# Kernel tuning notes

Measured on AMD Instinct MI355X. Metric: run time of the kernel, lower is better.

Reference implementation:

```python
import math
import jax, jax.numpy as jnp
import numpy as np

NUM_BUCKETS = 32
MAX_DISTANCE = 128
HEADS = 16
D_MODEL = 1024
SEQ = 1024
BATCH = 4
SCALE = (D_MODEL // HEADS) ** -0.5  # applied ONLY to the relative-position bias, per the source


def _rel_pos_bucket_causal(seq_len):
    """Causal T5 relative-position bucket: ret[i, j] for query i, key j."""
    pos = jnp.arange(seq_len)
    # rel_pos = k - q ; n = -rel_pos = q - k, clamped at 0 (causal branch)
    n = jnp.maximum(pos[:, None] - pos[None, :], 0)
    max_exact = NUM_BUCKETS // 2  # 16
    # log-spaced buckets for large distances; guard n>=1 to avoid log(0)
    val_large = max_exact + (
        jnp.log(jnp.maximum(n, 1).astype(jnp.float32) / max_exact)
        / math.log(MAX_DISTANCE / max_exact)
        * (NUM_BUCKETS - max_exact)
    ).astype(jnp.int32)
    val_large = jnp.minimum(val_large, NUM_BUCKETS - 1)
    return jnp.where(n < max_exact, n, val_large)  # [i, j] int32


def setup_inputs() -> dict:
    key = jax.random.key(0)
    ks = jax.random.split(key, 6)
    s = 0.02
    return {
        "x": jax.random.normal(ks[0], (BATCH, SEQ, D_MODEL), jnp.float32),
        "Wq": jax.random.normal(ks[1], (D_MODEL, D_MODEL), jnp.float32) * s,
        "bq": jnp.zeros((D_MODEL,), jnp.float32),
        "Wk": jax.random.normal(ks[2], (D_MODEL, D_MODEL), jnp.float32) * s,
        "bk": jnp.zeros((D_MODEL,), jnp.float32),
        "Wv": jax.random.normal(ks[3], (D_MODEL, D_MODEL), jnp.float32) * s,
        "bv": jnp.zeros((D_MODEL,), jnp.float32),
        "Wo": jax.random.normal(ks[4], (D_MODEL, D_MODEL), jnp.float32) * s,
        "bo": jnp.zeros((D_MODEL,), jnp.float32),
        "rel_emb": jax.random.normal(ks[5], (NUM_BUCKETS, HEADS), jnp.float32) * s,
    }


def reference(x, Wq, bq, Wk, bk, Wv, bv, Wo, bo, rel_emb):
    b, n, d = x.shape
    h, hd = HEADS, d // HEADS
    # projections (torch Linear: x @ W^T + b)
    q = (x @ Wq.T + bq).reshape(b, n, h, hd).transpose(0, 2, 1, 3)  # bhnd
    k = (x @ Wk.T + bk).reshape(b, n, h, hd).transpose(0, 2, 1, 3)
    v = (x @ Wv.T + bv).reshape(b, n, h, hd).transpose(0, 2, 1, 3)
    # unscaled dot-product scores (module does not scale q.k)
    sim = jnp.einsum("bhid,bhjd->bhij", q, k)
    # T5 relative-position bias, scaled by head_dim^-0.5
    rp_bucket = _rel_pos_bucket_causal(n)            # [i, j]
    bias = rel_emb[rp_bucket]                        # [i, j, h]
    sim = sim + jnp.transpose(bias, (2, 0, 1)) * SCALE  # broadcast over batch
    # additive causal mask (-inf above diagonal)
    i = jnp.arange(n)
    causal = jnp.where(i[None, :] > i[:, None], -jnp.inf, 0.0).astype(sim.dtype)
    sim = sim + causal
    attn = jax.nn.softmax(sim, axis=-1)
    out = jnp.einsum("bhij,bhjd->bhid", attn, v)
    out = out.transpose(0, 2, 1, 3).reshape(b, n, d)
    return out @ Wo.T + bo
```

## Files before the change

### kernel.cpp

```cpp
#include <hip/hip_runtime.h>
#include <hip/hip_bf16.h>
#include <stdint.h>

#define B_   4
#define SEQ_ 1024
#define DM   1024
#define H_   16
#define HD   64

typedef __bf16 bf16;
typedef __bf16 bf16x8 __attribute__((ext_vector_type(8)));
typedef __bf16 bf16x4v __attribute__((ext_vector_type(4)));
typedef float  f32x4 __attribute__((ext_vector_type(4)));

__device__ __forceinline__ void gl_lds16(const void* g, void* s_uniform) {
    __builtin_amdgcn_global_load_lds(
        (const __attribute__((address_space(1))) uint32_t*)g,
        (__attribute__((address_space(3))) uint32_t*)s_uniform,
        16, 0, 0);
}

__global__ __launch_bounds__(256) void prep_kernel(
    const float* __restrict__ x, const float* __restrict__ Wq,
    const float* __restrict__ Wk, const float* __restrict__ Wv,
    const float* __restrict__ Wo, const float* __restrict__ rel,
    bf16* __restrict__ xb, bf16* __restrict__ wqkvb, bf16* __restrict__ wob,
    float* __restrict__ biasT)
{
    int tid = blockIdx.x * 256 + threadIdx.x;
    int stride = gridDim.x * 256;

    for (int i = tid; i < (B_*SEQ_*DM)/4; i += stride) {
        float4 v = ((const float4*)x)[i];
        bf16x4v o; o[0]=(bf16)v.x; o[1]=(bf16)v.y; o[2]=(bf16)v.z; o[3]=(bf16)v.w;
        ((bf16x4v*)xb)[i] = o;
    }
    for (int i = tid; i < (3*DM*DM)/4; i += stride) {
        int n = i >> 8, k4 = i & 255;
        const float* src = (n < 1024) ? Wq : (n < 2048) ? Wk : Wv;
        float4 v = ((const float4*)(src + (size_t)(n & 1023) * DM))[k4];
        bf16x4v o; o[0]=(bf16)v.x; o[1]=(bf16)v.y; o[2]=(bf16)v.z; o[3]=(bf16)v.w;
        ((bf16x4v*)wqkvb)[i] = o;
    }
    for (int i = tid; i < (DM*DM)/4; i += stride) {
        float4 v = ((const float4*)Wo)[i];
        bf16x4v o; o[0]=(bf16)v.x; o[1]=(bf16)v.y; o[2]=(bf16)v.z; o[3]=(bf16)v.w;
        ((bf16x4v*)wob)[i] = o;
    }
    for (int i = tid; i < H_ * SEQ_; i += stride) {
        int h = i >> 10, dist = i & 1023;
        int bkt;
        if (dist < 16) {
            bkt = dist;
        } else {
            float r = logf((float)dist * (1.0f/16.0f)) / logf(8.0f) * 16.0f;
            int vb = 16 + (int)r;
            bkt = vb > 31 ? 31 : vb;
        }
        biasT[i] = rel[bkt * H_ + h] * 0.125f;
    }
}

template<int NT>
__global__ __launch_bounds__(256, 3) void gemm_ring(
    const bf16* __restrict__ Ag, const bf16* __restrict__ Bg,
    int ntx, int chunk,
    bf16* __restrict__ qb, bf16* __restrict__ kb, bf16* __restrict__ vtb,
    const float* __restrict__ bq, const float* __restrict__ bk,
    const float* __restrict__ bv)
{
    __shared__ __align__(16) bf16 tile[3][256 * 32];

    const int t = threadIdx.x;
    const int lane = t & 63, w = t >> 6;
    const int wr = w >> 1, wc = w & 1;
    const int row_l = lane & 15;
    const int lg = lane >> 4;

    int sw = (blockIdx.x & 7) * chunk + (blockIdx.x >> 3);
    int tx = sw % ntx, ty = sw / ntx;
    const int m0 = ty * 128, n0 = tx * 128;

    f32x4 acc[4][4] = {};

    auto STAGE = [&](int buf, int kt) {
        bf16* dst = &tile[buf][0];
        #pragma unroll
        for (int i = 0; i < 4; ++i) {
            int e = i * 2048 + t * 8;
            int r = e >> 5;
            int csw = ((t & 3) ^ (r & 3)) << 3;
            const bf16* src = (r < 128)
                ? (Ag + (long)(m0 + r) * 1024 + kt * 32 + csw)
                : (Bg + (long)(n0 + r - 128) * 1024 + kt * 32 + csw);
            gl_lds16(src, dst + i * 2048 + w * 512);
        }
    };

    auto COMPUTE = [&](int buf) {
        const bf16* bp = &tile[buf][0];
        bf16x8 af[4], bfr[4];
        #pragma unroll
        for (int m = 0; m < 4; ++m) {
            int ra = wr * 64 + m * 16 + row_l;
            af[m] = *(const bf16x8*)&bp[ra * 32 + ((lg ^ (ra & 3)) << 3)];
        }
        #pragma unroll
        for (int n = 0; n < 4; ++n) {
            int rb = 128 + wc * 64 + n * 16 + row_l;
            bfr[n] = *(const bf16x8*)&bp[rb * 32 + ((lg ^ (rb & 3)) << 3)];
        }
        #pragma unroll
        for (int m = 0; m < 4; ++m)
            #pragma unroll
            for (int n = 0; n < 4; ++n)
                acc[m][n] = __builtin_amdgcn_mfma_f32_16x16x32_bf16(
                    af[m], bfr[n], acc[m][n], 0, 0, 0);
    };

    STAGE(0, 0); STAGE(1, 1);
    asm volatile("s_waitcnt vmcnt(4)" ::: "memory");
    __builtin_amdgcn_s_barrier();

    int cb = 0;
    for (int kt = 0; kt < NT; ++kt) {
        int sb = cb - 1; if (sb < 0) sb += 3;
        if (kt + 2 < NT) STAGE(sb, kt + 2);
        COMPUTE(cb);
        if (kt + 2 < NT) { asm volatile("s_waitcnt vmcnt(4)" ::: "memory"); }
        else             { asm volatile("s_waitcnt vmcnt(0)" ::: "memory"); }
        __builtin_amdgcn_s_barrier();
        cb = (cb + 1 == 3) ? 0 : cb + 1;
    }

    const int rbase = (lane >> 4) * 4;
    #pragma unroll
    for (int m = 0; m < 4; ++m) {
        #pragma unroll
        for (int n = 0; n < 4; ++n) {
            #pragma unroll
            for (int g = 0; g < 4; ++g) {
                int gm = m0 + wr * 64 + m * 16 + rbase + g;
                int gn = n0 + wc * 64 + n * 16 + row_l;
                float v = acc[m][n][g];
                int which = gn >> 10, nn = gn & 1023;
                int h = nn >> 6, d = nn & 63;
                int b = gm >> 10, s = gm & 1023;
                const float* bias = (which == 0) ? bq : (which == 1) ? bk : bv;
                v += bias[nn];
                bf16 bv16 = (bf16)v;
                if (which == 0)
                    qb[((long)(b*H_ + h)*SEQ_ + s)*HD + d] = bv16;
                else if (which == 1)
                    kb[((long)(b*H_ + h)*SEQ_ + s)*HD + d] = bv16;
                else
                    vtb[((long)(b*H_ + h)*HD + d)*SEQ_ + s] = bv16;
            }
        }
    }
}

template<int MR, int NR, int MINW>
__global__ __launch_bounds__(512, MINW) void gemm2(
    const bf16* __restrict__ Ag, const bf16* __restrict__ Bg,
    int K, int ntx, int chunk,
    float* __restrict__ outp, const float* __restrict__ bo, int Nout)
{
    constexpr int BM = MR * 32;
    constexpr int BN = NR * 64;
    constexpr int NISS = (BM + BN) / 64;

    __shared__ __align__(16) bf16 tile[2][(BM + BN) * 64];

    const int t = threadIdx.x;
    const int lane = t & 63, w = t >> 6;
    const int wr = w >> 2, wc = w & 3;
    const int row_l = lane & 15;
    const int ksl = (lane >> 4) * 8;

    int sw = (blockIdx.x & 7) * chunk + (blockIdx.x >> 3);
    int tx = sw % ntx, ty = sw / ntx;
    const int m0 = ty * BM, n0 = tx * BN;

    f32x4 acc[MR][NR] = {};

    auto STAGE = [&](int buf, int kt) {
        #pragma unroll
        for (int i = 0; i < NISS; ++i) {
            int e = i * 4096 + t * 8;
            int r = e >> 6, c = e & 63;
            const bf16* src = (r < BM)
                ? (Ag + (long)(m0 + r) * K + kt * 64 + c)
                : (Bg + (long)(n0 + r - BM) * K + kt * 64 + c);
            gl_lds16(src, &tile[buf][i * 4096 + w * 512]);
        }
    };

    const int NT = K >> 6;

    STAGE(0, 0);
    asm volatile("s_waitcnt vmcnt(0)" ::: "memory");
    __builtin_amdgcn_s_barrier();

    int cur = 0;
    for (int kt = 0; kt < NT; ++kt) {
        if (kt + 1 < NT) STAGE(cur ^ 1, kt + 1);

        #pragma unroll
        for (int ks = 0; ks < 2; ++ks) {
            bf16x8 af[MR], bfr[NR];
            #pragma unroll
            for (int m = 0; m < MR; ++m)
                af[m] = *(const bf16x8*)&tile[cur][(wr*(BM/2) + m*16 + row_l)*64 + ks*32 + ksl];
            #pragma unroll
            for (int n = 0; n < NR; ++n)
                bfr[n] = *(const bf16x8*)&tile[cur][(BM + wc*(NR*16) + n*16 + row_l)*64 + ks*32 + ksl];
            #pragma unroll
            for (int m = 0; m < MR; ++m)
                #pragma unroll
                for (int n = 0; n < NR; ++n)
                    acc[m][n] = __builtin_amdgcn_mfma_f32_16x16x32_bf16(
                        af[m], bfr[n], acc[m][n], 0, 0, 0);
        }

        asm volatile("s_waitcnt vmcnt(0)" ::: "memory");
        __builtin_amdgcn_s_barrier();
        cur ^= 1;
    }

    const int rbase = (lane >> 4) * 4;
    #pragma unroll
    for (int m = 0; m < MR; ++m) {
        #pragma unroll
        for (int n = 0; n < NR; ++n) {
            #pragma unroll
            for (int g = 0; g < 4; ++g) {
                int gm = m0 + wr*(BM/2) + m*16 + rbase + g;
                int gn = n0 + wc*(NR*16) + n*16 + row_l;
                outp[(long)gm * Nout + gn] = acc[m][n][g] + bo[gn];
            }
        }
    }
}

#define PSTRIDE 72

__global__ __launch_bounds__(256, 3) void attn_kernel(
    const bf16* __restrict__ Qb, const bf16* __restrict__ Kb,
    const bf16* __restrict__ Vtb, const float* __restrict__ biasT,
    bf16* __restrict__ AO)
{
    __shared__ __align__(16) bf16 Ks[2][64 * 64];
    __shared__ __align__(16) bf16 Vs[2][64 * 64];
    __shared__ __align__(16) bf16 Ps[4][16 * PSTRIDE];
    __shared__ float biasS[SEQ_];

    int t = threadIdx.x;
    int lane = t & 63, w = t >> 6;

    int bid = blockIdx.x;
    int xcd = bid & 7;
    int widx = bid >> 3;
    int g = xcd * 8 + (widx >> 3);
    int pair = widx & 7;
    int qt_lo = pair, qt_hi = 15 - pair;
    int h = g & 15, b = g >> 4;

    int row_l = lane & 15;
    int ksl = (lane >> 4) * 8;
    int rbase = (lane >> 4) * 4;

    ((float4*)biasS)[t] = ((const float4*)(biasT + (long)h * SEQ_))[t];

    const bf16* Kbase = Kb + (long)g * SEQ_ * HD;
    const bf16* Vbase = Vtb + (long)g * HD * SEQ_;

    const bf16* QpA = Qb + ((long)g * SEQ_ + qt_lo * 64 + w * 16) * HD;
    const bf16* QpB = Qb + ((long)g * SEQ_ + qt_hi * 64 + w * 16) * HD;
    bf16x8 qA0 = *(const bf16x8*)&QpA[row_l * HD + ksl];
    bf16x8 qA1 = *(const bf16x8*)&QpA[row_l * HD + 32 + ksl];
    bf16x8 qB0 = *(const bf16x8*)&QpB[row_l * HD + ksl];
    bf16x8 qB1 = *(const bf16x8*)&QpB[row_l * HD + 32 + ksl];

    f32x4 oaccA[4] = {}, oaccB[4] = {};
    float lA[4] = {0.f, 0.f, 0.f, 0.f}, lB[4] = {0.f, 0.f, 0.f, 0.f};
    int irA[4], irB[4];
    #pragma unroll
    for (int q = 0; q < 4; ++q) {
        irA[q] = qt_lo * 64 + w * 16 + rbase + q;
        irB[q] = qt_hi * 64 + w * 16 + rbase + q;
    }

    int srow = w * 8 + (lane >> 3);
    int csw  = ((lane & 7) ^ (lane >> 3)) * 8;

    {
        int jt = 0;
        #pragma unroll
        for (int i = 0; i < 2; ++i) {
            int r = i * 32 + srow;
            gl_lds16(Kbase + (long)(jt*64 + r) * HD + csw, &Ks[0][i*2048 + w*512]);
            gl_lds16(Vbase + (long)r * SEQ_ + jt*64 + csw, &Vs[0][i*2048 + w*512]);
        }
    }
    __syncthreads();

    int cur = 0;
    for (int jt = 0; jt <= qt_hi; ++jt) {
        if (jt < qt_hi) {
            int nb = cur ^ 1, jn = jt + 1;
            #pragma unroll
            for (int i = 0; i < 2; ++i) {
                int r = i * 32 + srow;
                gl_lds16(Kbase + (long)(jn*64 + r) * HD + csw, &Ks[nb][i*2048 + w*512]);
                gl_lds16(Vbase + (long)r * SEQ_ + jn*64 + csw, &Vs[nb][i*2048 + w*512]);
            }
        }
        bool dolo = (jt <= qt_lo);

        f32x4 sA[4] = {}, sB[4] = {};
        __builtin_amdgcn_s_setprio(1);
        #pragma unroll
        for (int f = 0; f < 4; ++f) {
            int ra = f * 16 + row_l;
            int a0 = (ra * 64 + ksl)      ^ ((ra & 7) << 3);
            int a1 = (ra * 64 + 32 + ksl) ^ ((ra & 7) << 3);
            bf16x8 kf0 = *(const bf16x8*)&Ks[cur][a0];
            bf16x8 kf1 = *(const bf16x8*)&Ks[cur][a1];
            sB[f] = __builtin_amdgcn_mfma_f32_16x16x32_bf16(qB0, kf0, sB[f], 0,0,0);
            sB[f] = __builtin_amdgcn_mfma_f32_16x16x32_bf16(qB1, kf1, sB[f], 0,0,0);
            if (dolo) {
                sA[f] = __builtin_amdgcn_mfma_f32_16x16x32_bf16(qA0, kf0, sA[f], 0,0,0);
                sA[f] = __builtin_amdgcn_mfma_f32_16x16x32_bf16(qA1, kf1, sA[f], 0,0,0);
            }
        }
        __builtin_amdgcn_s_setprio(0);

        bf16x8 vf[4][2];
        #pragma unroll
        for (int f = 0; f < 4; ++f) {
            int ra = f * 16 + row_l;
            int a0 = (ra * 64 + ksl)      ^ ((ra & 7) << 3);
            int a1 = (ra * 64 + 32 + ksl) ^ ((ra & 7) << 3);
            vf[f][0] = *(const bf16x8*)&Vs[cur][a0];
            vf[f][1] = *(const bf16x8*)&Vs[cur][a1];
        }

        {
            #pragma unroll
            for (int f = 0; f < 4; ++f) {
                int j = jt * 64 + f * 16 + row_l;
                #pragma unroll
                for (int q = 0; q < 4; ++q) {
                    float sv = (j <= irB[q]) ? (sB[f][q] + biasS[irB[q] - j]) : -1e30f;
                    float p = __expf(sv);
                    lB[q] += p;
                    Ps[w][(rbase + q) * PSTRIDE + f * 16 + row_l] = (bf16)p;
                }
            }
            bf16x8 pf0 = *(const bf16x8*)&Ps[w][row_l * PSTRIDE + ksl];
            bf16x8 pf1 = *(const bf16x8*)&Ps[w][row_l * PSTRIDE + 32 + ksl];
            __builtin_amdgcn_s_setprio(1);
            #pragma unroll
            for (int db = 0; db < 4; ++db) {
                oaccB[db] = __builtin_amdgcn_mfma_f32_16x16x32_bf16(pf0, vf[db][0], oaccB[db], 0,0,0);
                oaccB[db] = __builtin_amdgcn_mfma_f32_16x16x32_bf16(pf1, vf[db][1], oaccB[db], 0,0,0);
            }
            __builtin_amdgcn_s_setprio(0);
        }

        if (dolo) {
            #pragma unroll
            for (int f = 0; f < 4; ++f) {
                int j = jt * 64 + f * 16 + row_l;
                #pragma unroll
                for (int q = 0; q < 4; ++q) {
                    float sv = (j <= irA[q]) ? (sA[f][q] + biasS[irA[q] - j]) : -1e30f;
                    float p = __expf(sv);
                    lA[q] += p;
                    Ps[w][(rbase + q) * PSTRIDE + f * 16 + row_l] = (bf16)p;
                }
            }
            bf16x8 pf0 = *(const bf16x8*)&Ps[w][row_l * PSTRIDE + ksl];
            bf16x8 pf1 = *(const bf16x8*)&Ps[w][row_l * PSTRIDE + 32 + ksl];
            __builtin_amdgcn_s_setprio(1);
            #pragma unroll
            for (int db = 0; db < 4; ++db) {
                oaccA[db] = __builtin_amdgcn_mfma_f32_16x16x32_bf16(pf0, vf[db][0], oaccA[db], 0,0,0);
                oaccA[db] = __builtin_amdgcn_mfma_f32_16x16x32_bf16(pf1, vf[db][1], oaccA[db], 0,0,0);
            }
            __builtin_amdgcn_s_setprio(0);
        }

        __syncthreads();
        cur ^= 1;
    }

    #pragma unroll
    for (int q = 0; q < 4; ++q) {
        float la = lA[q], lb = lB[q];
        #pragma unroll
        for (int off = 1; off < 16; off <<= 1) {
            la += __shfl_xor(la, off);
            lb += __shfl_xor(lb, off);
        }
        float invA = 1.0f / la;
        float invB = 1.0f / lb;
        long baseA = ((long)(b * SEQ_ + irA[q])) * DM + h * HD;
        long baseB = ((long)(b * SEQ_ + irB[q])) * DM + h * HD;
        #pragma unroll
        for (int db = 0; db < 4; ++db) {
            AO[baseA + db * 16 + row_l] = (bf16)(oaccA[db][q] * invA);
            AO[baseB + db * 16 + row_l] = (bf16)(oaccB[db][q] * invB);
        }
    }
}

extern "C" void kernel_launch(void* const* d_in, const int* in_sizes, int n_in,
                              void* d_out, int out_size, void* d_ws, size_t ws_size,
                              hipStream_t stream)
{
    const float* x   = (const float*)d_in[0];
    const float* Wq  = (const float*)d_in[1];
    const float* bq  = (const float*)d_in[2];
    const float* Wk  = (const float*)d_in[3];
    const float* bk  = (const float*)d_in[4];
    const float* Wv  = (const float*)d_in[5];
    const float* bv  = (const float*)d_in[6];
    const float* Wo  = (const float*)d_in[7];
    const float* bo  = (const float*)d_in[8];
    const float* rel = (const float*)d_in[9];
    float* out = (float*)d_out;

    char* ws = (char*)d_ws;
    bf16* xb    = (bf16*)ws;  ws += (size_t)B_*SEQ_*DM * 2;
    bf16* wqkvb = (bf16*)ws;  ws += (size_t)3*DM*DM * 2;
    bf16* wob   = (bf16*)ws;  ws += (size_t)DM*DM * 2;
    float* biasT= (float*)ws; ws += (size_t)H_*SEQ_ * 4;
    bf16* Qb    = (bf16*)ws;  ws += (size_t)B_*H_*SEQ_*HD * 2;
    bf16* Kb2   = (bf16*)ws;  ws += (size_t)B_*H_*SEQ_*HD * 2;
    bf16* Vtb   = (bf16*)ws;  ws += (size_t)B_*H_*SEQ_*HD * 2;
    bf16* AO    = (bf16*)ws;  ws += (size_t)B_*SEQ_*DM * 2;

    prep_kernel<<<2048, 256, 0, stream>>>(x, Wq, Wk, Wv, Wo, rel,
                                          xb, wqkvb, wob, biasT);

    gemm_ring<32><<<768, 256, 0, stream>>>(
        xb, wqkvb, 24, 96,
        Qb, Kb2, Vtb, bq, bk, bv);

    attn_kernel<<<512, 256, 0, stream>>>(Qb, Kb2, Vtb, biasT, AO);

    gemm2<4, 2, 4><<<256, 512, 0, stream>>>(
        AO, wob, DM, 8, 32,
        out, bo, DM);
}
```

Measured before the change: 106.2 us.

## Stage V-transpose epilogue through LDS, retile QKV swizzle, use ring GEMM for output

The QKV GEMM now maps blocks to 2D tile regions per XCD for better L2 locality. Its V-tile epilogue is restaged through swizzled LDS so the transposed V store goes out as 16-byte vectors instead of scattered 2-byte writes. The output projection drops the 512-thread double-buffered gemm2 and uses a new 3-stage ring-buffer GEMM with 128x64 tiles and 512 blocks. In exchange the V epilogue adds an extra barrier and LDS traffic, and the output kernel changes its occupancy and tile shape.

```diff
diff --git a/kernel.cpp b/kernel.cpp
--- a/kernel.cpp
+++ b/kernel.cpp
@@ -11,6 +11,7 @@
 typedef __bf16 bf16;
 typedef __bf16 bf16x8 __attribute__((ext_vector_type(8)));
 typedef __bf16 bf16x4v __attribute__((ext_vector_type(4)));
+typedef __bf16 bf16x2 __attribute__((ext_vector_type(2)));
 typedef float  f32x4 __attribute__((ext_vector_type(4)));
 
 __device__ __forceinline__ void gl_lds16(const void* g, void* s_uniform) {
@@ -64,7 +65,6 @@
 template<int NT>
 __global__ __launch_bounds__(256, 3) void gemm_ring(
     const bf16* __restrict__ Ag, const bf16* __restrict__ Bg,
-    int ntx, int chunk,
     bf16* __restrict__ qb, bf16* __restrict__ kb, bf16* __restrict__ vtb,
     const float* __restrict__ bq, const float* __restrict__ bk,
     const float* __restrict__ bv)
@@ -77,8 +77,10 @@
     const int row_l = lane & 15;
     const int lg = lane >> 4;
 
-    int sw = (blockIdx.x & 7) * chunk + (blockIdx.x >> 3);
-    int tx = sw % ntx, ty = sw / ntx;
+    int xcd = blockIdx.x & 7;
+    int idx = blockIdx.x >> 3;
+    int ty = (xcd >> 1) * 8 + idx / 12;
+    int tx = (xcd & 1) * 12 + idx % 12;
     const int m0 = ty * 128, n0 = tx * 128;
 
     f32x4 acc[4][4] = {};
@@ -134,110 +136,145 @@
     }
 
     const int rbase = (lane >> 4) * 4;
+
+    if (n0 < 2048) {
+        #pragma unroll
+        for (int m = 0; m < 4; ++m) {
+            #pragma unroll
+            for (int n = 0; n < 4; ++n) {
+                #pragma unroll
+                for (int g = 0; g < 4; ++g) {
+                    int gm = m0 + wr * 64 + m * 16 + rbase + g;
+                    int gn = n0 + wc * 64 + n * 16 + row_l;
+                    int which = gn >> 10, nn = gn & 1023;
+                    int h = nn >> 6, d = nn & 63;
+                    int b = gm >> 10, s = gm & 1023;
+                    float v = acc[m][n][g] + ((which == 0) ? bq[nn] : bk[nn]);
+                    bf16 bv16 = (bf16)v;
+                    if (which == 0)
+                        qb[((long)(b*H_ + h)*SEQ_ + s)*HD + d] = bv16;
+                    else
+                        kb[((long)(b*H_ + h)*SEQ_ + s)*HD + d] = bv16;
+                }
+            }
+        }
+    } else {
+        bf16* lt = &tile[0][0];
+        #pragma unroll
+        for (int m = 0; m < 4; ++m) {
+            #pragma unroll
+            for (int n = 0; n < 4; ++n) {
+                int nl = wc * 64 + n * 16 + row_l;
+                int mlb = wr * 64 + m * 16 + rbase;
+                float bvv = bv[(n0 & 1023) + nl];
+                #pragma unroll
+                for (int g2 = 0; g2 < 2; ++g2) {
+                    bf16x2 pk;
+                    pk[0] = (bf16)(acc[m][n][2*g2]     + bvv);
+                    pk[1] = (bf16)(acc[m][n][2*g2 + 1] + bvv);
+                    int ml = mlb + 2 * g2;
+                    int byte = nl * 256 + ((ml * 2) ^ ((nl & 15) << 4));
+                    *(bf16x2*)((char*)lt + byte) = pk;
+                }
+            }
+        }
+        __syncthreads();
+        {
+            int nl = t >> 1, sc = t & 1;
+            int nn = (n0 & 1023) + nl;
+            int h = nn >> 6, d = nn & 63;
+            int b = m0 >> 10, s0 = (m0 & 1023) + sc * 64;
+            bf16* dst = vtb + ((long)(b*H_ + h)*HD + d)*SEQ_ + s0;
+            #pragma unroll
+            for (int i = 0; i < 8; ++i) {
+                int byte = nl * 256 + ((sc * 128 + i * 16) ^ ((nl & 15) << 4));
+                *(float4*)(dst + i * 8) = *(const float4*)((char*)lt + byte);
+            }
+        }
+    }
+}
+
+template<int NT>
+__global__ __launch_bounds__(256, 2) void gemm_ring_o(
+    const bf16* __restrict__ Ag, const bf16* __restrict__ Bg,
+    float* __restrict__ outp, const float* __restrict__ bo)
+{
+    __shared__ __align__(16) bf16 tile[3][192 * 32];
+
+    const int t = threadIdx.x;
+    const int lane = t & 63, w = t >> 6;
+    const int wr = w >> 1, wc = w & 1;
+    const int row_l = lane & 15;
+    const int lg = lane >> 4;
+
+    int xcd = blockIdx.x & 7;
+    int idx = blockIdx.x >> 3;
+    int ty = (xcd >> 1) * 8 + (idx >> 3);
+    int tx = (xcd & 1) * 8 + (idx & 7);
+    const int m0 = ty * 128, n0 = tx * 64;
+
+    f32x4 acc[4][2] = {};
+
+    auto STAGE = [&](int buf, int kt) {
+        bf16* dst = &tile[buf][0];
+        #pragma unroll
+        for (int i = 0; i < 3; ++i) {
+            int e = i * 2048 + t * 8;
+            int r = e >> 5;
+            int csw = ((t & 3) ^ (r & 3)) << 3;
+            const bf16* src = (r < 128)
+                ? (Ag + (long)(m0 + r) * 1024 + kt * 32 + csw)
+                : (Bg + (long)(n0 + r - 128) * 1024 + kt * 32 + csw);
+            gl_lds16(src, dst + i * 2048 + w * 512);
+        }
+    };
+
+    auto COMPUTE = [&](int buf) {
+        const bf16* bp = &tile[buf][0];
+        bf16x8 af[4], bfr[2];
+        #pragma unroll
+        for (int m = 0; m < 4; ++m) {
+            int ra = wr * 64 + m * 16 + row_l;
+            af[m] = *(const bf16x8*)&bp[ra * 32 + ((lg ^ (ra & 3)) << 3)];
+        }
+        #pragma unroll
+        for (int n = 0; n < 2; ++n) {
+            int rb = 128 + wc * 32 + n * 16 + row_l;
+            bfr[n] = *(const bf16x8*)&bp[rb * 32 + ((lg ^ (rb & 3)) << 3)];
+        }
+        #pragma unroll
+        for (int m = 0; m < 4; ++m)
+            #pragma unroll
+            for (int n = 0; n < 2; ++n)
+                acc[m][n] = __builtin_amdgcn_mfma_f32_16x16x32_bf16(
+                    af[m], bfr[n], acc[m][n], 0, 0, 0);
+    };
+
+    STAGE(0, 0); STAGE(1, 1);
+    asm volatile("s_waitcnt vmcnt(3)" ::: "memory");
+    __builtin_amdgcn_s_barrier();
+
+    int cb = 0;
+    for (int kt = 0; kt < NT; ++kt) {
+        int sb = cb - 1; if (sb < 0) sb += 3;
+        if (kt + 2 < NT) STAGE(sb, kt + 2);
+        COMPUTE(cb);
+        if (kt + 2 < NT) { asm volatile("s_waitcnt vmcnt(3)" ::: "memory"); }
+        else             { asm volatile("s_waitcnt vmcnt(0)" ::: "memory"); }
+        __builtin_amdgcn_s_barrier();
+        cb = (cb + 1 == 3) ? 0 : cb + 1;
+    }
+
+    const int rbase = (lane >> 4) * 4;
     #pragma unroll
     for (int m = 0; m < 4; ++m) {
         #pragma unroll
-        for (int n = 0; n < 4; ++n) {
+        for (int n = 0; n < 2; ++n) {
             #pragma unroll
             for (int g = 0; g < 4; ++g) {
                 int gm = m0 + wr * 64 + m * 16 + rbase + g;
-                int gn = n0 + wc * 64 + n * 16 + row_l;
-                float v = acc[m][n][g];
-                int which = gn >> 10, nn = gn & 1023;
-                int h = nn >> 6, d = nn & 63;
-                int b = gm >> 10, s = gm & 1023;
-                const float* bias = (which == 0) ? bq : (which == 1) ? bk : bv;
-                v += bias[nn];
-                bf16 bv16 = (bf16)v;
-                if (which == 0)
-                    qb[((long)(b*H_ + h)*SEQ_ + s)*HD + d] = bv16;
-                else if (which == 1)
-                    kb[((long)(b*H_ + h)*SEQ_ + s)*HD + d] = bv16;
-                else
-                    vtb[((long)(b*H_ + h)*HD + d)*SEQ_ + s] = bv16;
-            }
-        }
-    }
-}
-
-template<int MR, int NR, int MINW>
-__global__ __launch_bounds__(512, MINW) void gemm2(
-    const bf16* __restrict__ Ag, const bf16* __restrict__ Bg,
-    int K, int ntx, int chunk,
-    float* __restrict__ outp, const float* __restrict__ bo, int Nout)
-{
-    constexpr int BM = MR * 32;
-    constexpr int BN = NR * 64;
-    constexpr int NISS = (BM + BN) / 64;
-
-    __shared__ __align__(16) bf16 tile[2][(BM + BN) * 64];
-
-    const int t = threadIdx.x;
-    const int lane = t & 63, w = t >> 6;
-    const int wr = w >> 2, wc = w & 3;
-    const int row_l = lane & 15;
-    const int ksl = (lane >> 4) * 8;
-
-    int sw = (blockIdx.x & 7) * chunk + (blockIdx.x >> 3);
-    int tx = sw % ntx, ty = sw / ntx;
-    const int m0 = ty * BM, n0 = tx * BN;
-
-    f32x4 acc[MR][NR] = {};
-
-    auto STAGE = [&](int buf, int kt) {
-        #pragma unroll
-        for (int i = 0; i < NISS; ++i) {
-            int e = i * 4096 + t * 8;
-            int r = e >> 6, c = e & 63;
-            const bf16* src = (r < BM)
-                ? (Ag + (long)(m0 + r) * K + kt * 64 + c)
-                : (Bg + (long)(n0 + r - BM) * K + kt * 64 + c);
-            gl_lds16(src, &tile[buf][i * 4096 + w * 512]);
-        }
-    };
-
-    const int NT = K >> 6;
-
-    STAGE(0, 0);
-    asm volatile("s_waitcnt vmcnt(0)" ::: "memory");
-    __builtin_amdgcn_s_barrier();
-
-    int cur = 0;
-    for (int kt = 0; kt < NT; ++kt) {
-        if (kt + 1 < NT) STAGE(cur ^ 1, kt + 1);
-
-        #pragma unroll
-        for (int ks = 0; ks < 2; ++ks) {
-            bf16x8 af[MR], bfr[NR];
-            #pragma unroll
-            for (int m = 0; m < MR; ++m)
-                af[m] = *(const bf16x8*)&tile[cur][(wr*(BM/2) + m*16 + row_l)*64 + ks*32 + ksl];
-            #pragma unroll
-            for (int n = 0; n < NR; ++n)
-                bfr[n] = *(const bf16x8*)&tile[cur][(BM + wc*(NR*16) + n*16 + row_l)*64 + ks*32 + ksl];
-            #pragma unroll
-            for (int m = 0; m < MR; ++m)
-                #pragma unroll
-                for (int n = 0; n < NR; ++n)
-                    acc[m][n] = __builtin_amdgcn_mfma_f32_16x16x32_bf16(
-                        af[m], bfr[n], acc[m][n], 0, 0, 0);
-        }
-
-        asm volatile("s_waitcnt vmcnt(0)" ::: "memory");
-        __builtin_amdgcn_s_barrier();
-        cur ^= 1;
-    }
-
-    const int rbase = (lane >> 4) * 4;
-    #pragma unroll
-    for (int m = 0; m < MR; ++m) {
-        #pragma unroll
-        for (int n = 0; n < NR; ++n) {
-            #pragma unroll
-            for (int g = 0; g < 4; ++g) {
-                int gm = m0 + wr*(BM/2) + m*16 + rbase + g;
-                int gn = n0 + wc*(NR*16) + n*16 + row_l;
-                outp[(long)gm * Nout + gn] = acc[m][n][g] + bo[gn];
+                int gn = n0 + wc * 32 + n * 16 + row_l;
+                outp[(long)gm * DM + gn] = acc[m][n][g] + bo[gn];
             }
         }
     }
@@ -446,12 +483,9 @@
                                           xb, wqkvb, wob, biasT);
 
     gemm_ring<32><<<768, 256, 0, stream>>>(
-        xb, wqkvb, 24, 96,
-        Qb, Kb2, Vtb, bq, bk, bv);
+        xb, wqkvb, Qb, Kb2, Vtb, bq, bk, bv);
 
     attn_kernel<<<512, 256, 0, stream>>>(Qb, Kb2, Vtb, biasT, AO);
 
-    gemm2<4, 2, 4><<<256, 512, 0, stream>>>(
-        AO, wob, DM, 8, 32,
-        out, bo, DM);
-}
+    gemm_ring_o<32><<<512, 256, 0, stream>>>(AO, wob, out, bo);
+}
```

After: 100.6 us. 1.06x faster.
